# Performance work log

Hardware: AMD Instinct MI355X
Metric: run time of the kernel (lower is better)

Reference implementation:

```python
import jax, jax.numpy as jnp
import numpy as np
from jax import lax

HW = 256 * 256      # patch h*w
WINDOW = 65536
STRIDE = 32768


def _conv2d(x, w, b, stride, pad):
    y = lax.conv_general_dilated(x, w, (stride, stride), [(pad, pad), (pad, pad)],
                                 dimension_numbers=('NCHW', 'OIHW', 'NCHW'))
    return y + b[None, :, None, None]


def _fcn(x, w1, b1, w2, b2, w3, b3, w4, b4):
    x = jax.nn.relu(_conv2d(x, w1, b1, 6, 6))
    x = jax.nn.relu(_conv2d(x, w2, b2, 4, 4))
    x = jax.nn.relu(_conv2d(x, w3, b3, 2, 2))
    x = jax.nn.relu(_conv2d(x, w4, b4, 1, 1))
    return x


def _avgpool2(x):
    # torch AvgPool2d(2,2,padding=1), count_include_pad=True -> sum window / 4
    s = lax.reduce_window(x, 0.0, lax.add, (1, 1, 2, 2), (1, 1, 2, 2),
                          [(0, 0), (0, 0), (1, 1), (1, 1)])
    return s * 0.25


def _cca(x, qw, qb, kw, kb, vw, vb, gamma):
    B, C, H, W = x.shape
    q = _conv2d(x, qw, qb, 1, 0)   # (B, C//8, H, W)
    k = _conv2d(x, kw, kb, 1, 0)
    v = _conv2d(x, vw, vb, 1, 0)   # (B, C, H, W)
    # column (height-axis) energies with -inf on the diagonal (self position)
    eH = jnp.einsum('bchw,bcgw->bhwg', q, k)                     # (B,H,W,H')
    eH = jnp.where(jnp.eye(H, dtype=bool)[:, None, :], -jnp.inf, eH)
    # row (width-axis) energies
    eW = jnp.einsum('bchw,bchv->bhwv', q, k)                     # (B,H,W,W')
    att = jax.nn.softmax(jnp.concatenate([eH, eW], axis=3), axis=3)
    outH = jnp.einsum('bcgw,bhwg->bchw', v, att[..., :H])
    outW = jnp.einsum('bchv,bhwv->bchw', v, att[..., H:])
    return gamma * (outH + outW) + x


def _forward(x, f0_w1, f0_b1, f0_w2, f0_b2, f0_w3, f0_b3, f0_w4, f0_b4,
             f1_w1, f1_b1, f1_w2, f1_b2, f1_w3, f1_b3, f1_w4, f1_b4,
             qw, qb, kw, kb, vw, vb, gamma, cls_w, cls_b):
    B, nc, L = x.shape
    need = HW - L % HW                 # torch pads a full extra block when L % hw == 0
    xp = jnp.pad(x, ((0, 0), (0, 0), (0, need)))
    nw = (L + need - WINDOW) // STRIDE + 1
    idx = jnp.arange(nw)[:, None] * STRIDE + jnp.arange(WINDOW)[None, :]
    wins = xp[:, 0, :][:, idx]                      # (B, nw, WINDOW) ~ torch unfold
    # torch does a raw reshape (nw,1,h,w) -> (1,1,h*w,nw); row-major reshape matches
    c_in = wins.reshape(B, 1, HW, nw)
    c0 = _fcn(c_in, f0_w1, f0_b1, f0_w2, f0_b2, f0_w3, f0_b3, f0_w4, f0_b4)
    c1 = _fcn(_avgpool2(c_in), f1_w1, f1_b1, f1_w2, f1_b2, f1_w3, f1_b3, f1_w4, f1_b4)
    a0 = _cca(c0, qw, qb, kw, kb, vw, vb, gamma)
    a1 = _cca(c1, qw, qb, kw, kb, vw, vb, gamma)   # 'twoheadfcn' reuses cca_attn0
    feat = jnp.concatenate([a0.mean(axis=(2, 3)), a1.mean(axis=(2, 3))], axis=1)
    return feat @ cls_w.T + cls_b                   # dropout = identity at eval


def setup_inputs():
    key = jax.random.key(0)
    ks = jax.random.split(key, 32)

    def he(k, shape):
        fan_in = int(np.prod(shape[1:]))
        return (jax.random.normal(k, shape) / np.sqrt(fan_in)).astype(jnp.float32)

    inp = {'x': jax.random.uniform(ks[0], (2, 1, 4194304), dtype=jnp.float32)}
    shapes = [(64, 1, 12, 12), (128, 64, 8, 8), (256, 128, 5, 5), (128, 256, 3, 3)]
    for pre, off in (('f0', 1), ('f1', 9)):
        for i, s in enumerate(shapes):
            inp[f'{pre}_w{i+1}'] = he(ks[off + 2 * i], s)
            inp[f'{pre}_b{i+1}'] = (0.01 * jax.random.normal(ks[off + 2 * i + 1], (s[0],))).astype(jnp.float32)
    inp['qw'] = he(ks[17], (16, 128, 1, 1)); inp['qb'] = jnp.zeros((16,), jnp.float32)
    inp['kw'] = he(ks[18], (16, 128, 1, 1)); inp['kb'] = jnp.zeros((16,), jnp.float32)
    inp['vw'] = he(ks[19], (128, 128, 1, 1)); inp['vb'] = jnp.zeros((128,), jnp.float32)
    inp['gamma'] = jnp.full((1,), 0.1, jnp.float32)
    inp['cls_w'] = he(ks[20], (2, 256)); inp['cls_b'] = jnp.zeros((2,), jnp.float32)
    return inp


def reference(x, f0_w1, f0_b1, f0_w2, f0_b2, f0_w3, f0_b3, f0_w4, f0_b4,
              f1_w1, f1_b1, f1_w2, f1_b2, f1_w3, f1_b3, f1_w4, f1_b4,
              qw, qb, kw, kb, vw, vb, gamma, cls_w, cls_b):
    return _forward(x, f0_w1, f0_b1, f0_w2, f0_b2, f0_w3, f0_b3, f0_w4, f0_b4,
                    f1_w1, f1_b1, f1_w2, f1_b2, f1_w3, f1_b3, f1_w4, f1_b4,
                    qw, qb, kw, kb, vw, vb, gamma, cls_w, cls_b)
```

## Files before the change

kernel.cpp:

```cpp
#include <hip/hip_runtime.h>
#include <math.h>

#define BLK 256
static const long LX = 4194304;

typedef __bf16 bf16x8 __attribute__((ext_vector_type(8)));
typedef float  f32x4  __attribute__((ext_vector_type(4)));
typedef unsigned short u16;

__device__ __forceinline__ void bf16split(float x, u16& h, u16& l) {
    unsigned u = __float_as_uint(x);
    unsigned hr = (u + 0x7fffu + ((u >> 16) & 1u)) >> 16;
    h = (u16)hr;
    float hf = __uint_as_float(hr << 16);
    float r = x - hf;
    unsigned v = __float_as_uint(r);
    unsigned lr2 = (v + 0x7fffu + ((v >> 16) & 1u)) >> 16;
    l = (u16)lr2;
}

__device__ __forceinline__ float cin_val(const float* __restrict__ x, long xbase, int h, int w) {
    if ((unsigned)h >= 65536u || (unsigned)w >= 129u) return 0.f;
    long flat = (long)h * 129 + w;
    int n = (int)(flat >> 16);
    int q = (int)(flat & 65535);
    long pos = (long)n * 32768 + q;
    return (pos < LX) ? x[xbase + pos] : 0.f;
}

template<int TOC>
__global__ __launch_bounds__(BLK)
void conv1_synth_k(const float* __restrict__ x, const float* __restrict__ wr1,
                   const float* __restrict__ bias, u16* __restrict__ outh, u16* __restrict__ outl,
                   int B, int Cout, int Hout, int Wout) {
    const int K = 12, S = 6, P = 6;
    long spatial = (long)B * Hout * Wout;
    long idx = (long)blockIdx.x * BLK + threadIdx.x;
    if (idx >= spatial) return;
    int wo = (int)(idx % Wout);
    long t = idx / Wout;
    int ho = (int)(t % Hout);
    int b  = (int)(t / Hout);
    int oc0 = blockIdx.y * TOC;
    float acc[TOC];
#pragma unroll
    for (int i = 0; i < TOC; i++) acc[i] = bias[oc0 + i];
    long xbase = (long)b * LX;
    int h0 = ho * S - P, w0 = wo * S - P;
    for (int kh = 0; kh < K; kh++) {
        int h = h0 + kh;
        for (int kw = 0; kw < K; kw++) {
            int w = w0 + kw;
            float v = cin_val(x, xbase, h, w);
            const float* wp = wr1 + (kh * K + kw) * Cout + oc0;
#pragma unroll
            for (int i = 0; i < TOC; i++) acc[i] = fmaf(v, wp[i], acc[i]);
        }
    }
    u16* oph = outh + idx * Cout + oc0;
    u16* opl = outl + idx * Cout + oc0;
#pragma unroll
    for (int i4 = 0; i4 < TOC / 4; i4++) {
        u16 hx, hy, hz, hw2, la, lb, lc, ld;
        bf16split(fmaxf(acc[i4*4+0], 0.f), hx, la);
        bf16split(fmaxf(acc[i4*4+1], 0.f), hy, lb);
        bf16split(fmaxf(acc[i4*4+2], 0.f), hz, lc);
        bf16split(fmaxf(acc[i4*4+3], 0.f), hw2, ld);
        *(ushort4*)(oph + i4 * 4) = make_ushort4(hx, hy, hz, hw2);
        *(ushort4*)(opl + i4 * 4) = make_ushort4(la, lb, lc, ld);
    }
}

template<int TOC>
__global__ __launch_bounds__(BLK)
void conv1_plane_k(const float* __restrict__ in, const float* __restrict__ wr1,
                   const float* __restrict__ bias, u16* __restrict__ outh, u16* __restrict__ outl,
                   int B, int Hin, int Win, int Cout, int Hout, int Wout) {
    const int K = 12, S = 6, P = 6;
    long spatial = (long)B * Hout * Wout;
    long idx = (long)blockIdx.x * BLK + threadIdx.x;
    if (idx >= spatial) return;
    int wo = (int)(idx % Wout);
    long t = idx / Wout;
    int ho = (int)(t % Hout);
    int b  = (int)(t / Hout);
    int oc0 = blockIdx.y * TOC;
    float acc[TOC];
#pragma unroll
    for (int i = 0; i < TOC; i++) acc[i] = bias[oc0 + i];
    const float* inb = in + (long)b * Hin * Win;
    int h0 = ho * S - P, w0 = wo * S - P;
    for (int kh = 0; kh < K; kh++) {
        int h = h0 + kh;
        bool hok = (unsigned)h < (unsigned)Hin;
        const float* row = inb + (long)h * Win;
        for (int kw = 0; kw < K; kw++) {
            int w = w0 + kw;
            float v = (hok && (unsigned)w < (unsigned)Win) ? row[w] : 0.f;
            const float* wp = wr1 + (kh * K + kw) * Cout + oc0;
#pragma unroll
            for (int i = 0; i < TOC; i++) acc[i] = fmaf(v, wp[i], acc[i]);
        }
    }
    u16* oph = outh + idx * Cout + oc0;
    u16* opl = outl + idx * Cout + oc0;
#pragma unroll
    for (int i4 = 0; i4 < TOC / 4; i4++) {
        u16 hx, hy, hz, hw2, la, lb, lc, ld;
        bf16split(fmaxf(acc[i4*4+0], 0.f), hx, la);
        bf16split(fmaxf(acc[i4*4+1], 0.f), hy, lb);
        bf16split(fmaxf(acc[i4*4+2], 0.f), hz, lc);
        bf16split(fmaxf(acc[i4*4+3], 0.f), hw2, ld);
        *(ushort4*)(oph + i4 * 4) = make_ushort4(hx, hy, hz, hw2);
        *(ushort4*)(opl + i4 * 4) = make_ushort4(la, lb, lc, ld);
    }
}

__global__ __launch_bounds__(BLK)
void avgpool_synth_k(const float* __restrict__ x, float* __restrict__ out, int B) {
    const int Ho = 32769, Wo = 65;
    long total = (long)B * Ho * Wo;
    long idx = (long)blockIdx.x * BLK + threadIdx.x;
    if (idx >= total) return;
    int w2 = (int)(idx % Wo);
    long t = idx / Wo;
    int p2 = (int)(t % Ho);
    int b  = (int)(t / Ho);
    long xbase = (long)b * LX;
    float s = 0.f;
#pragma unroll
    for (int dh = 0; dh < 2; dh++)
#pragma unroll
        for (int dw = 0; dw < 2; dw++)
            s += cin_val(x, xbase, 2 * p2 - 1 + dh, 2 * w2 - 1 + dw);
    out[idx] = 0.25f * s;
}

__global__ __launch_bounds__(BLK)
void reorder_w_k(const float* __restrict__ w, float* __restrict__ wrT,
                 int Cout, int Cin, int K2) {
    long total = (long)Cout * Cin * K2;
    long t = (long)blockIdx.x * BLK + threadIdx.x;
    if (t >= total) return;
    int khw = (int)(t % K2);
    long r = t / K2;
    int ic = (int)(r % Cin);
    int oc = (int)(r / Cin);
    wrT[((long)khw * Cin + ic) * Cout + oc] = w[t];
}

__global__ __launch_bounds__(BLK)
void reorder_ws_k(const float* __restrict__ w, u16* __restrict__ wh, u16* __restrict__ wl,
                  int Cout, int Cin, int Kk) {
    long total = (long)Cout * Cin * Kk * Kk;
    long t = (long)blockIdx.x * BLK + threadIdx.x;
    if (t >= total) return;
    int kw = (int)(t % Kk);
    long r = t / Kk;
    int kh = (int)(r % Kk); r /= Kk;
    int ic = (int)(r % Cin);
    int oc = (int)(r / Cin);
    long dst = (long)oc * (Cin * Kk * Kk) + (long)(kh * Kk + kw) * Cin + ic;
    u16 h, l; bf16split(w[t], h, l);
    wh[dst] = h; wl[dst] = l;
}

struct MJob {
    const u16* Ah; const u16* Al; const u16* Wh; const u16* Wl;
    const float* bias; float* out; float* part;
    int Hin, Win, Cin, cshift, Cout, K, S, P, Hout, Wout, relu, nks;
    long total; int nbx; int Ktot;
};

__global__ __launch_bounds__(256)
void mgemm2_k(MJob j0, MJob j1, int split) {
    __shared__ u16 lds[2][4][128 * 32];
    MJob j = j0;
    int bid = blockIdx.x;
    if (bid >= split) { j = j1; bid -= split; }
    const int bx = bid % j.nbx;
    int r2 = bid / j.nbx;
    const int nocb = j.Cout >> 7;
    const int ocb = (r2 % nocb) << 7;
    const int ks  = r2 / nocb;
    const int tid = threadIdx.x;
    const long spbase = (long)bx * 128;
    const int nchunk = j.Ktot >> 5;
    const int cbeg = (ks * nchunk) / j.nks;
    const int cend = ((ks + 1) * nchunk) / j.nks;

    const int sr = tid >> 1;
    const int sh = (tid & 1) << 4;
    long ssp = spbase + sr;
    const bool sval = ssp < j.total;
    long tt = sval ? ssp : 0;
    const int swo = (int)(tt % j.Wout); tt /= j.Wout;
    const int sho = (int)(tt % j.Hout);
    const int sb  = (int)(tt / j.Hout);
    const int sh0 = sho * j.S - j.P, sw0 = swo * j.S - j.P;
    const long ibase = (long)sb * j.Hin * j.Win;
    const long wbase = (long)(ocb + sr) * j.Ktot + sh;
    const int so = sr * 32 + sh;

    uint4 rA0, rA1, rL0, rL1, rB0, rB1, rM0, rM1;
    auto fetch = [&](int c) {
        int p0 = c << 5;
        int khw = p0 >> j.cshift;
        int ic0 = p0 - (khw << j.cshift);
        int kh = khw / j.K, kw = khw - kh * j.K;
        int h = sh0 + kh, w = sw0 + kw;
        bool ok = sval && (unsigned)h < (unsigned)j.Hin && (unsigned)w < (unsigned)j.Win;
        uint4 z = make_uint4(0u, 0u, 0u, 0u);
        const long e = (ibase + (long)h * j.Win + w) * j.Cin + ic0 + sh;
        rA0 = ok ? *(const uint4*)(j.Ah + e)     : z;
        rA1 = ok ? *(const uint4*)(j.Ah + e + 8) : z;
        rL0 = ok ? *(const uint4*)(j.Al + e)     : z;
        rL1 = ok ? *(const uint4*)(j.Al + e + 8) : z;
        const long we = wbase + p0;
        rB0 = *(const uint4*)(j.Wh + we);
        rB1 = *(const uint4*)(j.Wh + we + 8);
        rM0 = *(const uint4*)(j.Wl + we);
        rM1 = *(const uint4*)(j.Wl + we + 8);
    };
    auto store = [&](int buf) {
        *(uint4*)&lds[buf][0][so] = rA0; *(uint4*)&lds[buf][0][so + 8] = rA1;
        *(uint4*)&lds[buf][1][so] = rL0; *(uint4*)&lds[buf][1][so + 8] = rL1;
        *(uint4*)&lds[buf][2][so] = rB0; *(uint4*)&lds[buf][2][so + 8] = rB1;
        *(uint4*)&lds[buf][3][so] = rM0; *(uint4*)&lds[buf][3][so + 8] = rM1;
    };

    const int lane = tid & 63;
    const int wid = tid >> 6;
    const int wm = (wid >> 1) << 6, wn = (wid & 1) << 6;
    const int lr = lane & 15;
    const int lk = (lane >> 4) << 3;

    f32x4 acc[4][4];
    if (j.nks == 1) {
#pragma unroll
        for (int fn = 0; fn < 4; fn++) {
            float b = j.bias[ocb + wn + fn * 16 + lr];
#pragma unroll
            for (int fm = 0; fm < 4; fm++) { f32x4 v = {b, b, b, b}; acc[fm][fn] = v; }
        }
    } else {
#pragma unroll
        for (int fm = 0; fm < 4; fm++)
#pragma unroll
            for (int fn = 0; fn < 4; fn++) { f32x4 v = {0.f, 0.f, 0.f, 0.f}; acc[fm][fn] = v; }
    }

    fetch(cbeg); store(0);
    __syncthreads();

    for (int c = cbeg; c < cend; c++) {
        const int cur = (c - cbeg) & 1, nxt = cur ^ 1;
        const bool more = (c + 1 < cend);
        if (more) fetch(c + 1);
        const u16* Ahs = &lds[cur][0][0];
        const u16* Als = &lds[cur][1][0];
        const u16* Bhs = &lds[cur][2][0];
        const u16* Bls = &lds[cur][3][0];
        bf16x8 aH[4], aL[4], bH[4], bL[4];
#pragma unroll
        for (int f = 0; f < 4; f++) {
            aH[f] = *(const bf16x8*)(Ahs + (wm + f * 16 + lr) * 32 + lk);
            aL[f] = *(const bf16x8*)(Als + (wm + f * 16 + lr) * 32 + lk);
            bH[f] = *(const bf16x8*)(Bhs + (wn + f * 16 + lr) * 32 + lk);
            bL[f] = *(const bf16x8*)(Bls + (wn + f * 16 + lr) * 32 + lk);
        }
#pragma unroll
        for (int fm = 0; fm < 4; fm++)
#pragma unroll
            for (int fn = 0; fn < 4; fn++) {
                acc[fm][fn] = __builtin_amdgcn_mfma_f32_16x16x32_bf16(aL[fm], bH[fn], acc[fm][fn], 0, 0, 0);
                acc[fm][fn] = __builtin_amdgcn_mfma_f32_16x16x32_bf16(aH[fm], bL[fn], acc[fm][fn], 0, 0, 0);
                acc[fm][fn] = __builtin_amdgcn_mfma_f32_16x16x32_bf16(aH[fm], bH[fn], acc[fm][fn], 0, 0, 0);
            }
        if (more) store(nxt);
        __syncthreads();
    }

    const int row0 = (lane >> 4) << 2;
    if (j.nks == 1) {
#pragma unroll
        for (int fm = 0; fm < 4; fm++) {
#pragma unroll
            for (int q = 0; q < 4; q++) {
                long sp = spbase + wm + fm * 16 + row0 + q;
                if (sp < j.total) {
                    float* op = j.out + sp * j.Cout + ocb + wn + lr;
#pragma unroll
                    for (int fn = 0; fn < 4; fn++) {
                        float v = acc[fm][fn][q];
                        if (j.relu) v = fmaxf(v, 0.f);
                        op[fn * 16] = v;
                    }
                }
            }
        }
    } else {
        float* pb = j.part + ((long)ks * j.total) * j.Cout;
#pragma unroll
        for (int fm = 0; fm < 4; fm++) {
#pragma unroll
            for (int q = 0; q < 4; q++) {
                long sp = spbase + wm + fm * 16 + row0 + q;
                if (sp < j.total) {
                    float* op = pb + sp * j.Cout + ocb + wn + lr;
#pragma unroll
                    for (int fn = 0; fn < 4; fn++) op[fn * 16] = acc[fm][fn][q];
                }
            }
        }
    }
}

struct CJob {
    const float* part; const float* bias;
    float* outf; u16* outh; u16* outl;
    long n; int C; int nks; int relu;
};

__global__ __launch_bounds__(BLK)
void combine2m_k(CJob a, CJob b) {
    long q0 = a.n * (long)a.C / 4, q1 = b.n * (long)b.C / 4;
    long id = (long)blockIdx.x * BLK + threadIdx.x;
    CJob j; long f4;
    if (id < q0) { j = a; f4 = id * 4; }
    else if (id < q0 + q1) { j = b; f4 = (id - q0) * 4; }
    else return;
    long stride = j.n * (long)j.C;
    int cb = (int)(f4 % j.C);
    float4 s = *(const float4*)(j.bias + cb);
    for (int ss = 0; ss < j.nks; ss++) {
        float4 p = *(const float4*)(j.part + ss * stride + f4);
        s.x += p.x; s.y += p.y; s.z += p.z; s.w += p.w;
    }
    if (j.relu) {
        s.x = fmaxf(s.x, 0.f); s.y = fmaxf(s.y, 0.f);
        s.z = fmaxf(s.z, 0.f); s.w = fmaxf(s.w, 0.f);
    }
    if (j.outf) *(float4*)(j.outf + f4) = s;
    if (j.outh) {
        u16 hx, hy, hz, hw2, la, lb, lc, ld;
        bf16split(s.x, hx, la); bf16split(s.y, hy, lb);
        bf16split(s.z, hz, lc); bf16split(s.w, hw2, ld);
        *(ushort4*)(j.outh + f4) = make_ushort4(hx, hy, hz, hw2);
        *(ushort4*)(j.outl + f4) = make_ushort4(la, lb, lc, ld);
    }
}

__global__ __launch_bounds__(256)
void qk2_k(const float* __restrict__ in,
           const float* __restrict__ qw, const float* __restrict__ qb,
           const float* __restrict__ kw2, const float* __restrict__ kb2,
           float* __restrict__ outq, float* __restrict__ outk, long total) {
    const float* w    = blockIdx.y ? kw2 : qw;
    const float* bias = blockIdx.y ? kb2 : qb;
    float* out        = blockIdx.y ? outk : outq;
    __shared__ float As[64 * 132];
    __shared__ float Ws[128 * 16];
    int tid = threadIdx.x;
    long spbase = (long)blockIdx.x * 64;
    int r = tid >> 2;
    int cpart = (tid & 3) << 5;
    long sp = spbase + r;
    bool ok = sp < total;
    const float* ip = in + sp * 128 + cpart;
#pragma unroll
    for (int jj = 0; jj < 8; jj++) {
        float4 v = ok ? *(const float4*)(ip + jj * 4) : make_float4(0.f, 0.f, 0.f, 0.f);
        *(float4*)&As[r * 132 + cpart + jj * 4] = v;
    }
    for (int t = tid; t < 2048; t += 256) Ws[(t & 127) * 16 + (t >> 7)] = w[t];
    __syncthreads();
    int ocp = (tid & 3) << 2;
    float acc[4] = {bias[ocp], bias[ocp + 1], bias[ocp + 2], bias[ocp + 3]};
    for (int ic = 0; ic < 128; ic++) {
        float a = As[r * 132 + ic];
#pragma unroll
        for (int jj = 0; jj < 4; jj++) acc[jj] = fmaf(a, Ws[ic * 16 + ocp + jj], acc[jj]);
    }
    if (ok) {
#pragma unroll
        for (int jj = 0; jj < 4; jj++) out[sp * 16 + ocp + jj] = acc[jj];
    }
}

struct AJob {
    const float* q; const float* kk; const float* v;
    float* pacc; float* pm; float* pl;
    int B, H, W, nrt, ns, ntile;
};

__global__ __launch_bounds__(256)
void cca_part_k(AJob j0, AJob j1, int n0) {
    const int RT = 16, TG = 64;
    __shared__ float lbuf[8192];
    __shared__ float mlb2[32];
    float* kls    = lbuf;
    float* sc     = lbuf + 1088;
    float* scales = lbuf + 2176;
    AJob j = j0;
    int bid = blockIdx.x;
    if (bid >= n0) { j = j1; bid -= n0; }
    int rt = bid % j.nrt; int t = bid / j.nrt;
    int ksp = t % j.ns; t /= j.ns;
    int w = t % j.W; int b = t / j.W;
    const int H = j.H, W = j.W;
    const int tid = threadIdx.x;
    const int r = tid >> 4, l16 = tid & 15;
    const int h = rt * RT + r;
    const int hc = (h < H) ? h : (H - 1);
    const long colbase = (long)b * H * W + w;
    const long rowbase = ((long)b * H + hc) * W;

    float qreg[16];
    {
        const float* qp = j.q + (rowbase + w) * 16;
#pragma unroll
        for (int jj = 0; jj < 4; jj++) {
            float4 t4 = *(const float4*)(qp + 4 * jj);
            qreg[4*jj] = t4.x; qreg[4*jj+1] = t4.y; qreg[4*jj+2] = t4.z; qreg[4*jj+3] = t4.w;
        }
    }
    const int lane6 = tid & 63;
    const int wid = tid >> 6;
    const int c2 = lane6 << 1;
    float accv[16][2];
#pragma unroll
    for (int i = 0; i < 16; i++) { accv[i][0] = 0.f; accv[i][1] = 0.f; }

    float m = -INFINITY, l = 0.f;
    const int gp = l16 * 4;

    const int tbeg = (ksp * j.ntile) / j.ns;
    const int tend = ((ksp + 1) * j.ntile) / j.ns;
    for (int tt2 = tbeg; tt2 < tend; tt2++) {
        const int g0 = tt2 * TG;
        {
            int kr = tid >> 2, kc = (tid & 3) << 2;
            int gg = g0 + kr;
            float4 kv = make_float4(0.f, 0.f, 0.f, 0.f);
            if (gg < H) kv = *(const float4*)(j.kk + (colbase + (long)gg * W) * 16 + kc);
            kls[kr * 17 + kc + 0] = kv.x; kls[kr * 17 + kc + 1] = kv.y;
            kls[kr * 17 + kc + 2] = kv.z; kls[kr * 17 + kc + 3] = kv.w;
        }
        __syncthreads();
        float sloc[4];
#pragma unroll
        for (int i = 0; i < 4; i++) {
            int gg = g0 + gp + i;
            float d = 0.f;
#pragma unroll
            for (int c = 0; c < 16; c++) d = fmaf(qreg[c], kls[(gp + i) * 17 + c], d);
            sloc[i] = (gg >= H || gg == h) ? -INFINITY : d;
        }
        float tmax = fmaxf(fmaxf(sloc[0], sloc[1]), fmaxf(sloc[2], sloc[3]));
#pragma unroll
        for (int off = 1; off < 16; off <<= 1) tmax = fmaxf(tmax, __shfl_xor(tmax, off, 16));
        float mt = fmaxf(m, tmax);
        float scale = __expf(m - mt);
        float ps = 0.f;
#pragma unroll
        for (int i = 0; i < 4; i++) {
            float p = __expf(sloc[i] - mt);
            ps += p;
            sc[r * 68 + gp + i] = p;
        }
#pragma unroll
        for (int off = 1; off < 16; off <<= 1) ps += __shfl_xor(ps, off, 16);
        l = l * scale + ps;
        m = mt;
        if (l16 == 0) scales[r] = scale;
        __syncthreads();
        {
            float4 sA = *(const float4*)&scales[0];
            float4 sB = *(const float4*)&scales[4];
            float4 sC = *(const float4*)&scales[8];
            float4 sD = *(const float4*)&scales[12];
            float sarr[16] = {sA.x,sA.y,sA.z,sA.w, sB.x,sB.y,sB.z,sB.w,
                              sC.x,sC.y,sC.z,sC.w, sD.x,sD.y,sD.z,sD.w};
#pragma unroll
            for (int row = 0; row < 16; row++) {
                accv[row][0] *= sarr[row];
                accv[row][1] *= sarr[row];
            }
#pragma unroll
            for (int s = 0; s < 2; s++) {
                const int k0 = (wid << 4) + (s << 3);
                float2 v2[8];
#pragma unroll
                for (int kq = 0; kq < 8; kq++) {
                    int gg = g0 + k0 + kq;
                    if (gg >= H) gg = H - 1;
                    v2[kq] = *(const float2*)(j.v + (colbase + (long)gg * W) * 128 + c2);
                }
#pragma unroll
                for (int row = 0; row < 16; row++) {
                    float4 pA = *(const float4*)&sc[row * 68 + k0];
                    float4 pB = *(const float4*)&sc[row * 68 + k0 + 4];
                    accv[row][0] = fmaf(pA.x, v2[0].x, accv[row][0]);
                    accv[row][1] = fmaf(pA.x, v2[0].y, accv[row][1]);
                    accv[row][0] = fmaf(pA.y, v2[1].x, accv[row][0]);
                    accv[row][1] = fmaf(pA.y, v2[1].y, accv[row][1]);
                    accv[row][0] = fmaf(pA.z, v2[2].x, accv[row][0]);
                    accv[row][1] = fmaf(pA.z, v2[2].y, accv[row][1]);
                    accv[row][0] = fmaf(pA.w, v2[3].x, accv[row][0]);
                    accv[row][1] = fmaf(pA.w, v2[3].y, accv[row][1]);
                    accv[row][0] = fmaf(pB.x, v2[4].x, accv[row][0]);
                    accv[row][1] = fmaf(pB.x, v2[4].y, accv[row][1]);
                    accv[row][0] = fmaf(pB.y, v2[5].x, accv[row][0]);
                    accv[row][1] = fmaf(pB.y, v2[5].y, accv[row][1]);
                    accv[row][0] = fmaf(pB.z, v2[6].x, accv[row][0]);
                    accv[row][1] = fmaf(pB.z, v2[6].y, accv[row][1]);
                    accv[row][0] = fmaf(pB.w, v2[7].x, accv[row][0]);
                    accv[row][1] = fmaf(pB.w, v2[7].y, accv[row][1]);
                }
            }
        }
        __syncthreads();
    }
    if (ksp == 0) {
        float sw[3];
        float twmax = -INFINITY;
#pragma unroll
        for (int jj = 0; jj < 3; jj++) {
            sw[jj] = -INFINITY;
            if (jj < W) {
                const float* kp = j.kk + (rowbase + jj) * 16;
                float d = 0.f;
#pragma unroll
                for (int c = 0; c < 16; c++) d = fmaf(qreg[c], kp[c], d);
                sw[jj] = d;
                twmax = fmaxf(twmax, d);
            }
        }
        float mt = fmaxf(m, twmax);
        float scale = __expf(m - mt);
        l *= scale;
#pragma unroll
        for (int jj = 0; jj < 3; jj++) {
            if (jj < W) {
                float p = __expf(sw[jj] - mt);
                l += p;
                if (l16 == 0) sc[r * 68 + jj] = p;
            }
        }
        m = mt;
        if (l16 == 0) scales[r] = scale;
    }
    if (l16 == 0) { mlb2[2 * r] = m; mlb2[2 * r + 1] = l; }
    __syncthreads();
    if (ksp == 0) {
        float4 sA = *(const float4*)&scales[0];
        float4 sB = *(const float4*)&scales[4];
        float4 sC = *(const float4*)&scales[8];
        float4 sD = *(const float4*)&scales[12];
        float sarr[16] = {sA.x,sA.y,sA.z,sA.w, sB.x,sB.y,sB.z,sB.w,
                          sC.x,sC.y,sC.z,sC.w, sD.x,sD.y,sD.z,sD.w};
#pragma unroll
        for (int row = 0; row < 16; row++) {
            accv[row][0] *= sarr[row];
            accv[row][1] *= sarr[row];
            int hr = rt * RT + row;
            int hcr = (hr < H) ? hr : (H - 1);
            long rb = ((long)b * H + hcr) * W;
#pragma unroll
            for (int jj = 0; jj < 3; jj++) {
                if (jj < W) {
                    float p = sc[row * 68 + jj];
                    float2 vv = *(const float2*)(j.v + (rb + jj) * 128 + c2);
                    accv[row][0] = fmaf(p, vv.x, accv[row][0]);
                    accv[row][1] = fmaf(p, vv.y, accv[row][1]);
                }
            }
        }
    }
    __syncthreads();
#pragma unroll
    for (int row = 0; row < 16; row++) {
        *(float2*)&lbuf[(wid << 11) + (row << 7) + c2] = make_float2(accv[row][0], accv[row][1]);
    }
    __syncthreads();
    {
        int orow = tid >> 4, ocb = (tid & 15) << 3;
        int hr = rt * RT + orow;
        if (hr < H) {
            float4 r0 = make_float4(0.f, 0.f, 0.f, 0.f);
            float4 r1 = make_float4(0.f, 0.f, 0.f, 0.f);
#pragma unroll
            for (int wv = 0; wv < 4; wv++) {
                float4 a0 = *(const float4*)&lbuf[(wv << 11) + (orow << 7) + ocb];
                float4 a1 = *(const float4*)&lbuf[(wv << 11) + (orow << 7) + ocb + 4];
                r0.x += a0.x; r0.y += a0.y; r0.z += a0.z; r0.w += a0.w;
                r1.x += a1.x; r1.y += a1.y; r1.z += a1.z; r1.w += a1.w;
            }
            long qi = ((long)b * H + hr) * W + w;
            float* pp = j.pacc + (qi * j.ns + ksp) * 128 + ocb;
            *(float4*)pp       = r0;
            *(float4*)(pp + 4) = r1;
            if ((tid & 15) == 0) {
                j.pm[qi * j.ns + ksp] = mlb2[2 * orow];
                j.pl[qi * j.ns + ksp] = mlb2[2 * orow + 1];
            }
        }
    }
}

struct CCJob {
    const float* x; const float* pacc; const float* pm; const float* pl;
    float* out; long rows; int ns;
};

__global__ __launch_bounds__(BLK)
void cca_comb_k(CCJob a, CCJob b, const float* __restrict__ gamma) {
    long q0 = a.rows * 32, q1 = b.rows * 32;
    long id = (long)blockIdx.x * BLK + threadIdx.x;
    CCJob j; long lid;
    if (id < q0) { j = a; lid = id; }
    else if (id < q0 + q1) { j = b; lid = id - q0; }
    else return;
    long qi = lid >> 5;
    int c4 = (int)(lid & 31) << 2;
    int ns = j.ns;
    float M = -INFINITY;
    for (int s = 0; s < ns; s++) M = fmaxf(M, j.pm[qi * ns + s]);
    float L = 0.f;
    float4 acc = make_float4(0.f, 0.f, 0.f, 0.f);
    for (int s = 0; s < ns; s++) {
        float wgt = __expf(j.pm[qi * ns + s] - M);
        L += j.pl[qi * ns + s] * wgt;
        float4 p = *(const float4*)(j.pacc + (qi * ns + s) * 128 + c4);
        acc.x = fmaf(wgt, p.x, acc.x); acc.y = fmaf(wgt, p.y, acc.y);
        acc.z = fmaf(wgt, p.z, acc.z); acc.w = fmaf(wgt, p.w, acc.w);
    }
    float g = gamma[0] / L;
    float4 xr = *(const float4*)(j.x + qi * 128 + c4);
    float4 o = make_float4(g * acc.x + xr.x, g * acc.y + xr.y,
                           g * acc.z + xr.z, g * acc.w + xr.w);
    *(float4*)(j.out + qi * 128 + c4) = o;
}

__global__ __launch_bounds__(BLK)
void mean_part_k(const float* __restrict__ a, float* __restrict__ part, int HW, int NS) {
    int bx = blockIdx.x;
    int b = bx / NS, sc_ = bx % NS;
    int tid = threadIdx.x;
    int c = tid & 127, half = tid >> 7;
    int per = (HW + NS - 1) / NS;
    int s0 = sc_ * per, s1 = s0 + per; if (s1 > HW) s1 = HW;
    float acc = 0.f;
    for (int s = s0 + half; s < s1; s += 2) acc += a[((long)b * HW + s) * 128 + c];
    __shared__ float red[BLK];
    red[tid] = acc; __syncthreads();
    if (half == 0) part[(long)bx * 128 + c] = red[c] + red[c + 128];
}

__global__ __launch_bounds__(BLK)
void final2_k(const float* __restrict__ part0, const float* __restrict__ part1, int NS,
              const float* __restrict__ w, const float* __restrict__ bias,
              float* __restrict__ out, float hw0, float hw1) {
    __shared__ float feat[512];
    int tid = threadIdx.x;
    for (int t = tid; t < 512; t += BLK) {
        int b = t >> 8, c = t & 255;
        float s = 0.f;
        if (c < 128) {
            for (int ns = 0; ns < NS; ns++) s += part0[((long)b * NS + ns) * 128 + c];
            s /= hw0;
        } else {
            int cc = c - 128;
            for (int ns = 0; ns < NS; ns++) s += part1[((long)b * NS + ns) * 128 + cc];
            s /= hw1;
        }
        feat[t] = s;
    }
    __syncthreads();
    if (tid < 4) {
        int b = tid >> 1, jj = tid & 1;
        float s = bias[jj];
        for (int c = 0; c < 256; c++) s += feat[b * 256 + c] * w[jj * 256 + c];
        out[b * 2 + jj] = s;
    }
}

static inline long cdiv(long a, long b) { return (a + b - 1) / b; }

extern "C" void kernel_launch(void* const* d_in, const int* in_sizes, int n_in,
                              void* d_out, int out_size, void* d_ws, size_t ws_size,
                              hipStream_t stream) {
    const float* x     = (const float*)d_in[0];
    const float* f0w1  = (const float*)d_in[1];
    const float* f0b1  = (const float*)d_in[2];
    const float* f0w2  = (const float*)d_in[3];
    const float* f0b2  = (const float*)d_in[4];
    const float* f0w3  = (const float*)d_in[5];
    const float* f0b3  = (const float*)d_in[6];
    const float* f0w4  = (const float*)d_in[7];
    const float* f0b4  = (const float*)d_in[8];
    const float* f1w1  = (const float*)d_in[9];
    const float* f1b1  = (const float*)d_in[10];
    const float* f1w2  = (const float*)d_in[11];
    const float* f1b2  = (const float*)d_in[12];
    const float* f1w3  = (const float*)d_in[13];
    const float* f1b3  = (const float*)d_in[14];
    const float* f1w4  = (const float*)d_in[15];
    const float* f1b4  = (const float*)d_in[16];
    const float* qw    = (const float*)d_in[17];
    const float* qb    = (const float*)d_in[18];
    const float* kw    = (const float*)d_in[19];
    const float* kb    = (const float*)d_in[20];
    const float* vw    = (const float*)d_in[21];
    const float* vb    = (const float*)d_in[22];
    const float* gamma = (const float*)d_in[23];
    const float* clsw  = (const float*)d_in[24];
    const float* clsb  = (const float*)d_in[25];
    float* ws = (float*)d_ws;
    float* outp = (float*)d_out;

    const int B = 2;
    size_t off = 0;
    auto alloc = [&](size_t nfl) { size_t o = off; off += (nfl + 63) & ~(size_t)63; return o; };
    size_t o_pool = alloc((size_t)B * 32769 * 65);
    size_t o_A0h  = alloc((size_t)B * 10923 * 22 * 32);
    size_t o_A0l  = alloc((size_t)B * 10923 * 22 * 32);
    size_t o_A1h  = alloc((size_t)B * 5462 * 11 * 32);
    size_t o_A1l  = alloc((size_t)B * 5462 * 11 * 32);
    size_t o_B0h  = alloc((size_t)B * 2731 * 6 * 64);
    size_t o_B0l  = alloc((size_t)B * 2731 * 6 * 64);
    size_t o_c0   = alloc((size_t)B * 1366 * 3 * 128);
    size_t o_c1   = alloc((size_t)B * 683 * 2 * 128);
    size_t o_w1r0 = alloc((size_t)144 * 64);
    size_t o_w1r1 = alloc((size_t)144 * 64);
    size_t o_w2h0 = alloc((size_t)128 * 4096 / 2);
    size_t o_w2l0 = alloc((size_t)128 * 4096 / 2);
    size_t o_w2h1 = alloc((size_t)128 * 4096 / 2);
    size_t o_w2l1 = alloc((size_t)128 * 4096 / 2);
    size_t o_w3h0 = alloc((size_t)256 * 3200 / 2);
    size_t o_w3l0 = alloc((size_t)256 * 3200 / 2);
    size_t o_w3h1 = alloc((size_t)256 * 3200 / 2);
    size_t o_w3l1 = alloc((size_t)256 * 3200 / 2);
    size_t o_w4h0 = alloc((size_t)128 * 2304 / 2);
    size_t o_w4l0 = alloc((size_t)128 * 2304 / 2);
    size_t o_w4h1 = alloc((size_t)128 * 2304 / 2);
    size_t o_w4l1 = alloc((size_t)128 * 2304 / 2);
    size_t o_wvh  = alloc((size_t)128 * 128 / 2);
    size_t o_wvl  = alloc((size_t)128 * 128 / 2);
    size_t o_part = alloc((size_t)2 * (32772 + 8196) * 128);
    size_t need_main = off;
    size_t o_B1h = o_pool;
    size_t o_B1l = o_pool + (size_t)B * 1366 * 3 * 64;
    size_t sub = o_A0h;
    auto salloc = [&](size_t nfl) { size_t o = sub; sub += (nfl + 63) & ~(size_t)63; return o; };
    size_t o_C0h = salloc((size_t)B * 1366 * 3 * 128);
    size_t o_C0l = salloc((size_t)B * 1366 * 3 * 128);
    size_t o_C1h = salloc((size_t)B * 683 * 2 * 128);
    size_t o_C1l = salloc((size_t)B * 683 * 2 * 128);
    size_t o_c0h = salloc((size_t)B * 1366 * 3 * 64);
    size_t o_c0l = salloc((size_t)B * 1366 * 3 * 64);
    size_t o_c1h = salloc((size_t)B * 683 * 2 * 64);
    size_t o_c1l = salloc((size_t)B * 683 * 2 * 64);
    size_t o_q0  = salloc((size_t)B * 1366 * 3 * 16);
    size_t o_k0  = salloc((size_t)B * 1366 * 3 * 16);
    size_t o_v0  = salloc((size_t)B * 1366 * 3 * 128);
    size_t o_a0  = salloc((size_t)B * 1366 * 3 * 128);
    size_t o_q1  = salloc((size_t)B * 683 * 2 * 16);
    size_t o_k1  = salloc((size_t)B * 683 * 2 * 16);
    size_t o_v1  = salloc((size_t)B * 683 * 2 * 128);
    size_t o_a1  = salloc((size_t)B * 683 * 2 * 128);
    size_t o_p0  = salloc((size_t)B * 8 * 128);
    size_t o_p1  = salloc((size_t)B * 8 * 128);
    if (ws_size < need_main * sizeof(float)) {
        hipMemsetAsync(d_out, 0, (size_t)out_size * sizeof(float), stream);
        return;
    }
    auto U16 = [&](size_t o) { return (u16*)(ws + o); };

    {
        long tot = (long)B * 32769 * 65;
        avgpool_synth_k<<<dim3(cdiv(tot, BLK)), BLK, 0, stream>>>(x, ws + o_pool, B);
    }
    reorder_w_k<<<dim3(cdiv((long)64 * 144, BLK)), BLK, 0, stream>>>(f0w1, ws + o_w1r0, 64, 1, 144);
    reorder_w_k<<<dim3(cdiv((long)64 * 144, BLK)), BLK, 0, stream>>>(f1w1, ws + o_w1r1, 64, 1, 144);
    reorder_ws_k<<<dim3(cdiv((long)128 * 64 * 64, BLK)), BLK, 0, stream>>>(f0w2, U16(o_w2h0), U16(o_w2l0), 128, 64, 8);
    reorder_ws_k<<<dim3(cdiv((long)128 * 64 * 64, BLK)), BLK, 0, stream>>>(f1w2, U16(o_w2h1), U16(o_w2l1), 128, 64, 8);
    reorder_ws_k<<<dim3(cdiv((long)256 * 128 * 25, BLK)), BLK, 0, stream>>>(f0w3, U16(o_w3h0), U16(o_w3l0), 256, 128, 5);
    reorder_ws_k<<<dim3(cdiv((long)256 * 128 * 25, BLK)), BLK, 0, stream>>>(f1w3, U16(o_w3h1), U16(o_w3l1), 256, 128, 5);
    reorder_ws_k<<<dim3(cdiv((long)128 * 256 * 9, BLK)), BLK, 0, stream>>>(f0w4, U16(o_w4h0), U16(o_w4l0), 128, 256, 3);
    reorder_ws_k<<<dim3(cdiv((long)128 * 256 * 9, BLK)), BLK, 0, stream>>>(f1w4, U16(o_w4h1), U16(o_w4l1), 128, 256, 3);
    reorder_ws_k<<<dim3(cdiv((long)128 * 128, BLK)), BLK, 0, stream>>>(vw, U16(o_wvh), U16(o_wvl), 128, 128, 1);
    {
        long sp = (long)B * 5462 * 11;
        conv1_plane_k<32><<<dim3(cdiv(sp, BLK), 2), BLK, 0, stream>>>(
            ws + o_pool, ws + o_w1r1, f1b1, U16(o_A1h), U16(o_A1l), B, 32769, 65, 64, 5462, 11);
    }
    {
        long sp = (long)B * 10923 * 22;
        conv1_synth_k<32><<<dim3(cdiv(sp, BLK), 2), BLK, 0, stream>>>(
            x, ws + o_w1r0, f0b1, U16(o_A0h), U16(o_A0l), B, 64, 10923, 22);
    }

    float* partp = ws + o_part;
    auto mkM = [&](size_t ah, size_t al, size_t wh, size_t wl, const float* bias, float* out,
                   int Hin, int Win, int Cin, int cshift, int Cout,
                   int K, int S, int P, int Hout, int Wout, int relu) {
        MJob g;
        g.Ah = U16(ah); g.Al = U16(al); g.Wh = U16(wh); g.Wl = U16(wl);
        g.bias = bias; g.out = out; g.part = nullptr;
        g.Hin = Hin; g.Win = Win; g.Cin = Cin; g.cshift = cshift; g.Cout = Cout;
        g.K = K; g.S = S; g.P = P; g.Hout = Hout; g.Wout = Wout; g.relu = relu; g.nks = 1;
        g.total = (long)B * Hout * Wout;
        g.nbx = (int)((g.total + 127) / 128);
        g.Ktot = K * K * Cin;
        return g;
    };
    auto launchM = [&](MJob a, MJob b, int nks) {
        a.nks = nks; b.nks = nks;
        a.part = partp;
        b.part = partp + (size_t)nks * a.total * a.Cout;
        int na = a.nbx * (a.Cout >> 7) * nks;
        int nb = b.nbx * (b.Cout >> 7) * nks;
        mgemm2_k<<<dim3(na + nb), 256, 0, stream>>>(a, b, na);
    };

    {
        MJob a = mkM(o_A0h, o_A0l, o_w2h0, o_w2l0, f0b2, nullptr, 10923, 22, 64, 6, 128, 8, 4, 4, 2731, 6, 1);
        MJob b = mkM(o_A1h, o_A1l, o_w2h1, o_w2l1, f1b2, nullptr, 5462, 11, 64, 6, 128, 8, 4, 4, 1366, 3, 1);
        launchM(a, b, 2);
        CJob ca = {partp, f0b2, nullptr, U16(o_B0h), U16(o_B0l), a.total, 128, 2, 1};
        CJob cb = {partp + (size_t)2 * a.total * 128, f1b2, nullptr, U16(o_B1h), U16(o_B1l), b.total, 128, 2, 1};
        long n4 = (a.total * 128 + b.total * 128) / 4;
        combine2m_k<<<dim3(cdiv(n4, BLK)), BLK, 0, stream>>>(ca, cb);
    }
    {
        MJob a = mkM(o_B0h, o_B0l, o_w3h0, o_w3l0, f0b3, nullptr, 2731, 6, 128, 7, 256, 5, 2, 2, 1366, 3, 1);
        MJob b = mkM(o_B1h, o_B1l, o_w3h1, o_w3l1, f1b3, nullptr, 1366, 3, 128, 7, 256, 5, 2, 2, 683, 2, 1);
        launchM(a, b, 3);
        CJob ca = {partp, f0b3, nullptr, U16(o_C0h), U16(o_C0l), a.total, 256, 3, 1};
        CJob cb = {partp + (size_t)3 * a.total * 256, f1b3, nullptr, U16(o_C1h), U16(o_C1l), b.total, 256, 3, 1};
        long n4 = (a.total * 256 + b.total * 256) / 4;
        combine2m_k<<<dim3(cdiv(n4, BLK)), BLK, 0, stream>>>(ca, cb);
    }
    {
        MJob a = mkM(o_C0h, o_C0l, o_w4h0, o_w4l0, f0b4, nullptr, 1366, 3, 256, 8, 128, 3, 1, 1, 1366, 3, 1);
        MJob b = mkM(o_C1h, o_C1l, o_w4h1, o_w4l1, f1b4, nullptr, 683, 2, 256, 8, 128, 3, 1, 1, 683, 2, 1);
        launchM(a, b, 6);
        CJob ca = {partp, f0b4, ws + o_c0, U16(o_c0h), U16(o_c0l), a.total, 128, 6, 1};
        CJob cb = {partp + (size_t)6 * a.total * 128, f1b4, ws + o_c1, U16(o_c1h), U16(o_c1l), b.total, 128, 6, 1};
        long n4 = (a.total * 128 + b.total * 128) / 4;
        combine2m_k<<<dim3(cdiv(n4, BLK)), BLK, 0, stream>>>(ca, cb);
    }
    {
        long tot0 = (long)B * 1366 * 3;
        qk2_k<<<dim3(cdiv(tot0, 64), 2), 256, 0, stream>>>(
            ws + o_c0, qw, qb, kw, kb, ws + o_q0, ws + o_k0, tot0);
        long tot1 = (long)B * 683 * 2;
        qk2_k<<<dim3(cdiv(tot1, 64), 2), 256, 0, stream>>>(
            ws + o_c1, qw, qb, kw, kb, ws + o_q1, ws + o_k1, tot1);
    }
    {
        MJob a = mkM(o_c0h, o_c0l, o_wvh, o_wvl, vb, ws + o_v0, 1366, 3, 128, 7, 128, 1, 1, 0, 1366, 3, 0);
        MJob b = mkM(o_c1h, o_c1l, o_wvh, o_wvl, vb, ws + o_v1, 683, 2, 128, 7, 128, 1, 1, 0, 683, 2, 0);
        launchM(a, b, 1);
    }
    {
        const int nrt0 = 86, nrt1 = 43;
        const int ns0 = 6, ns1 = 3;
        const long rows0 = (long)B * 1366 * 3;
        const long rows1 = (long)B * 683 * 2;
        size_t pp = o_part;
        auto palloc = [&](size_t nfl) { size_t o = pp; pp += (nfl + 63) & ~(size_t)63; return o; };
        size_t o_pa0 = palloc((size_t)rows0 * ns0 * 128);
        size_t o_pm0 = palloc((size_t)rows0 * ns0);
        size_t o_pl0 = palloc((size_t)rows0 * ns0);
        size_t o_pa1 = palloc((size_t)rows1 * ns1 * 128);
        size_t o_pm1 = palloc((size_t)rows1 * ns1);
        size_t o_pl1 = palloc((size_t)rows1 * ns1);
        AJob a0 = { ws + o_q0, ws + o_k0, ws + o_v0,
                    ws + o_pa0, ws + o_pm0, ws + o_pl0, B, 1366, 3, nrt0, ns0, 22 };
        AJob a1 = { ws + o_q1, ws + o_k1, ws + o_v1,
                    ws + o_pa1, ws + o_pm1, ws + o_pl1, B, 683, 2, nrt1, ns1, 11 };
        int n0 = B * 3 * nrt0 * ns0;
        int n1 = B * 2 * nrt1 * ns1;
        cca_part_k<<<dim3(n0 + n1), 256, 0, stream>>>(a0, a1, n0);
        CCJob c0 = { ws + o_c0, ws + o_pa0, ws + o_pm0, ws + o_pl0, ws + o_a0, rows0, ns0 };
        CCJob c1 = { ws + o_c1, ws + o_pa1, ws + o_pm1, ws + o_pl1, ws + o_a1, rows1, ns1 };
        long tot = (rows0 + rows1) * 32;
        cca_comb_k<<<dim3(cdiv(tot, BLK)), BLK, 0, stream>>>(c0, c1, gamma);
    }
    mean_part_k<<<dim3(B * 8), BLK, 0, stream>>>(ws + o_a0, ws + o_p0, 1366 * 3, 8);
    mean_part_k<<<dim3(B * 8), BLK, 0, stream>>>(ws + o_a1, ws + o_p1, 683 * 2, 8);
    final2_k<<<dim3(1), BLK, 0, stream>>>(ws + o_p0, ws + o_p1, 8, clsw, clsb, outp,
                                          (float)(1366 * 3), (float)(683 * 2));
}
```

Before: 820.4 us.

## Rewrite first FCN conv as bf16x3 MFMA GEMM with LDS-staged input patch

Replaces the scalar FMA direct convolution for the branch-0 first layer (12x12 kernel, stride 6, one input channel) with an MFMA kernel. The kernel stages the synthesized unfolded input rows into shared memory as bf16 hi/lo pairs and runs an implicit GEMM over 144 taps padded to 160, using three bf16 MFMAs per tile to keep near-fp32 accuracy. A new weight reorder kernel packs the weights as split bf16. The goal is to cut the FMA-bound cost and the repeated global gathers of the old kernel, at the cost of complex index and boundary-masking logic and scalar 2-byte output stores.

```diff
diff --git a/kernel.cpp b/kernel.cpp
--- a/kernel.cpp
+++ b/kernel.cpp
@@ -28,47 +28,131 @@
     return (pos < LX) ? x[xbase + pos] : 0.f;
 }
 
-template<int TOC>
+__global__ __launch_bounds__(256)
+void conv1_mfma_k(const float* __restrict__ x, const u16* __restrict__ wbh,
+                  const u16* __restrict__ wbl, const float* __restrict__ bias,
+                  u16* __restrict__ outh, u16* __restrict__ outl) {
+    const long SPT = 240306;
+    __shared__ u16 ph[6400];
+    __shared__ u16 pl[6400];
+    const int tid = threadIdx.x;
+    const int b = blockIdx.y;
+    const long sp0 = (long)blockIdx.x * 128;
+    const long xbase = (long)b * LX;
+    const int ho_min = (int)sp0 / 22;
+    const int flat_start = (ho_min * 6 - 6) * 129 - 6;
+    for (int i = tid; i < 6400; i += 256) {
+        int flat = flat_start + i;
+        float v = 0.f;
+        if (flat >= 0 && flat < 65536 * 129) {
+            int n = flat >> 16, q = flat & 65535;
+            long pos = (long)n * 32768 + q;
+            if (pos < LX) v = x[xbase + pos];
+        }
+        u16 h, l; bf16split(v, h, l);
+        ph[i] = h; pl[i] = l;
+    }
+    __syncthreads();
+
+    const int lane = tid & 63, wid = tid >> 6;
+    const int lr = lane & 15;
+    const int lk = (lane >> 4) << 3;
+
+    int off0[2]; int wlo[2], whi[2];
+#pragma unroll
+    for (int fm = 0; fm < 2; fm++) {
+        int r = (wid << 5) + (fm << 4) + lr;
+        long spl = sp0 + r; if (spl >= SPT) spl = SPT - 1;
+        int sp = (int)spl;
+        int ho = sp / 22;
+        int wo = sp - ho * 22;
+        off0[fm] = (ho * 6 - 6) * 129 + (wo * 6 - 6) - flat_start;
+        wlo[fm] = (wo == 0) ? 1 : 0;
+        whi[fm] = (wo == 21) ? 1 : 0;
+    }
+
+    f32x4 acc[2][4];
+#pragma unroll
+    for (int fn = 0; fn < 4; fn++) {
+        float bv = bias[(fn << 4) + lr];
+#pragma unroll
+        for (int fm = 0; fm < 2; fm++) { f32x4 v = {bv, bv, bv, bv}; acc[fm][fn] = v; }
+    }
+
+    const bool zhi = (lk >= 16);
+#pragma unroll
+    for (int c = 0; c < 5; c++) {
+        bf16x8 bH[4], bL[4];
+#pragma unroll
+        for (int fn = 0; fn < 4; fn++) {
+            int oc = (fn << 4) + lr;
+            bH[fn] = *(const bf16x8*)(wbh + oc * 160 + (c << 5) + lk);
+            bL[fn] = *(const bf16x8*)(wbl + oc * 160 + (c << 5) + lk);
+        }
+        bf16x8 aH[2], aL[2];
+#pragma unroll
+        for (int fm = 0; fm < 2; fm++) {
+            union { bf16x8 v; u16 u[8]; } uh, ul;
+            if (c == 4 && zhi) {
+#pragma unroll
+                for (int jj = 0; jj < 8; jj++) { uh.u[jj] = 0; ul.u[jj] = 0; }
+            } else {
+                int t0 = (c << 5) + lk;
+                int kh0 = t0 / 12;
+                int r0 = t0 - kh0 * 12;
+                int jst = 12 - r0;
+                int base = off0[fm] + t0 + kh0 * 117;
+#pragma unroll
+                for (int jj = 0; jj < 8; jj++) {
+                    int wrapped = (jj >= jst) ? 1 : 0;
+                    int idx = base + jj + (wrapped ? 117 : 0);
+                    int kw = r0 + jj - (wrapped ? 12 : 0);
+                    int bad = (wlo[fm] & ((kw < 6) ? 1 : 0)) | (whi[fm] & ((kw > 8) ? 1 : 0));
+                    u16 hv = ph[idx];
+                    u16 lv = pl[idx];
+                    uh.u[jj] = bad ? (u16)0 : hv;
+                    ul.u[jj] = bad ? (u16)0 : lv;
+                }
+            }
+            aH[fm] = uh.v; aL[fm] = ul.v;
+        }
+#pragma unroll
+        for (int fm = 0; fm < 2; fm++)
+#pragma unroll
+            for (int fn = 0; fn < 4; fn++) {
+                acc[fm][fn] = __builtin_amdgcn_mfma_f32_16x16x32_bf16(aL[fm], bH[fn], acc[fm][fn], 0, 0, 0);
+                acc[fm][fn] = __builtin_amdgcn_mfma_f32_16x16x32_bf16(aH[fm], bL[fn], acc[fm][fn], 0, 0, 0);
+                acc[fm][fn] = __builtin_amdgcn_mfma_f32_16x16x32_bf16(aH[fm], bH[fn], acc[fm][fn], 0, 0, 0);
+            }
+    }
+    const int row0 = (lane >> 4) << 2;
+#pragma unroll
+    for (int fm = 0; fm < 2; fm++) {
+#pragma unroll
+        for (int q = 0; q < 4; q++) {
+            long sp = sp0 + (wid << 5) + (fm << 4) + row0 + q;
+            if (sp < SPT) {
+                long obase = ((long)b * SPT + sp) << 6;
+#pragma unroll
+                for (int fn = 0; fn < 4; fn++) {
+                    u16 h, l;
+                    bf16split(fmaxf(acc[fm][fn][q], 0.f), h, l);
+                    outh[obase + (fn << 4) + lr] = h;
+                    outl[obase + (fn << 4) + lr] = l;
+                }
+            }
+        }
+    }
+}
+
 __global__ __launch_bounds__(BLK)
-void conv1_synth_k(const float* __restrict__ x, const float* __restrict__ wr1,
-                   const float* __restrict__ bias, u16* __restrict__ outh, u16* __restrict__ outl,
-                   int B, int Cout, int Hout, int Wout) {
-    const int K = 12, S = 6, P = 6;
-    long spatial = (long)B * Hout * Wout;
-    long idx = (long)blockIdx.x * BLK + threadIdx.x;
-    if (idx >= spatial) return;
-    int wo = (int)(idx % Wout);
-    long t = idx / Wout;
-    int ho = (int)(t % Hout);
-    int b  = (int)(t / Hout);
-    int oc0 = blockIdx.y * TOC;
-    float acc[TOC];
-#pragma unroll
-    for (int i = 0; i < TOC; i++) acc[i] = bias[oc0 + i];
-    long xbase = (long)b * LX;
-    int h0 = ho * S - P, w0 = wo * S - P;
-    for (int kh = 0; kh < K; kh++) {
-        int h = h0 + kh;
-        for (int kw = 0; kw < K; kw++) {
-            int w = w0 + kw;
-            float v = cin_val(x, xbase, h, w);
-            const float* wp = wr1 + (kh * K + kw) * Cout + oc0;
-#pragma unroll
-            for (int i = 0; i < TOC; i++) acc[i] = fmaf(v, wp[i], acc[i]);
-        }
-    }
-    u16* oph = outh + idx * Cout + oc0;
-    u16* opl = outl + idx * Cout + oc0;
-#pragma unroll
-    for (int i4 = 0; i4 < TOC / 4; i4++) {
-        u16 hx, hy, hz, hw2, la, lb, lc, ld;
-        bf16split(fmaxf(acc[i4*4+0], 0.f), hx, la);
-        bf16split(fmaxf(acc[i4*4+1], 0.f), hy, lb);
-        bf16split(fmaxf(acc[i4*4+2], 0.f), hz, lc);
-        bf16split(fmaxf(acc[i4*4+3], 0.f), hw2, ld);
-        *(ushort4*)(oph + i4 * 4) = make_ushort4(hx, hy, hz, hw2);
-        *(ushort4*)(opl + i4 * 4) = make_ushort4(la, lb, lc, ld);
-    }
+void reorder_w1m_k(const float* __restrict__ w, u16* __restrict__ wh, u16* __restrict__ wl) {
+    int t = blockIdx.x * BLK + threadIdx.x;
+    if (t >= 64 * 160) return;
+    int tap = t % 160, oc = t / 160;
+    float v = (tap < 144) ? w[oc * 144 + tap] : 0.f;
+    u16 h, l; bf16split(v, h, l);
+    wh[t] = h; wl[t] = l;
 }
 
 template<int TOC>
@@ -732,8 +816,9 @@
     size_t o_B0l  = alloc((size_t)B * 2731 * 6 * 64);
     size_t o_c0   = alloc((size_t)B * 1366 * 3 * 128);
     size_t o_c1   = alloc((size_t)B * 683 * 2 * 128);
-    size_t o_w1r0 = alloc((size_t)144 * 64);
     size_t o_w1r1 = alloc((size_t)144 * 64);
+    size_t o_w1mh = alloc((size_t)64 * 160 / 2);
+    size_t o_w1ml = alloc((size_t)64 * 160 / 2);
     size_t o_w2h0 = alloc((size_t)128 * 4096 / 2);
     size_t o_w2l0 = alloc((size_t)128 * 4096 / 2);
     size_t o_w2h1 = alloc((size_t)128 * 4096 / 2);
@@ -782,8 +867,8 @@
         long tot = (long)B * 32769 * 65;
         avgpool_synth_k<<<dim3(cdiv(tot, BLK)), BLK, 0, stream>>>(x, ws + o_pool, B);
     }
-    reorder_w_k<<<dim3(cdiv((long)64 * 144, BLK)), BLK, 0, stream>>>(f0w1, ws + o_w1r0, 64, 1, 144);
     reorder_w_k<<<dim3(cdiv((long)64 * 144, BLK)), BLK, 0, stream>>>(f1w1, ws + o_w1r1, 64, 1, 144);
+    reorder_w1m_k<<<dim3(cdiv((long)64 * 160, BLK)), BLK, 0, stream>>>(f0w1, U16(o_w1mh), U16(o_w1ml));
     reorder_ws_k<<<dim3(cdiv((long)128 * 64 * 64, BLK)), BLK, 0, stream>>>(f0w2, U16(o_w2h0), U16(o_w2l0), 128, 64, 8);
     reorder_ws_k<<<dim3(cdiv((long)128 * 64 * 64, BLK)), BLK, 0, stream>>>(f1w2, U16(o_w2h1), U16(o_w2l1), 128, 64, 8);
     reorder_ws_k<<<dim3(cdiv((long)256 * 128 * 25, BLK)), BLK, 0, stream>>>(f0w3, U16(o_w3h0), U16(o_w3l0), 256, 128, 5);
@@ -797,9 +882,9 @@
             ws + o_pool, ws + o_w1r1, f1b1, U16(o_A1h), U16(o_A1l), B, 32769, 65, 64, 5462, 11);
     }
     {
-        long sp = (long)B * 10923 * 22;
-        conv1_synth_k<32><<<dim3(cdiv(sp, BLK), 2), BLK, 0, stream>>>(
-            x, ws + o_w1r0, f0b1, U16(o_A0h), U16(o_A0l), B, 64, 10923, 22);
+        int nbx = (int)cdiv(240306L, 128);
+        conv1_mfma_k<<<dim3(nbx, B), 256, 0, stream>>>(
+            x, U16(o_w1mh), U16(o_w1ml), f0b1, U16(o_A0h), U16(o_A0l));
     }
 
     float* partp = ws + o_part;
```

Result: faster. 748.5 us (-8.8%).
